# Kernel optimization log

Measured on AMD Instinct MI355X. Metric: run time of the kernel, lower is better.

The kernel has to match this reference:

```python
import jax, jax.numpy as jnp
import numpy as np

N = 100000
E = 640000
C = 128
NEG_SLOPE = 0.2


def _param(key, shape, scale=0.1):
    return jax.random.normal(key, shape, dtype=jnp.float32) * scale


def setup_inputs() -> dict:
    key = jax.random.key(0)
    ks = jax.random.split(key, 20)
    edge_index = jax.random.randint(ks[0], (2, E), 0, N, dtype=jnp.int32)
    emb = jax.random.normal(ks[1], (N, C), dtype=jnp.float32)  # node_embeddings.weight, a=1.0 normal
    d = {"edge_index": edge_index, "emb": emb}
    # per-layer GATv2Conv params: lin_l (W,b), lin_r (W,b), att vector, residual lin (no bias), out bias
    names = ["Wl", "bl", "Wr", "br", "att", "Wres", "bias"]
    shapes = [(C, C), (C,), (C, C), (C,), (C,), (C, C), (C,)]
    i = 2
    for layer in (1, 2):
        for nm, sh in zip(names, shapes):
            d[f"l{layer}_{nm}"] = _param(ks[i], sh)
            i += 1
    return d


def gatv2_layer(x, Wl, bl, Wr, br, att, Wres, bias, src, dst):
    # x: [N,C]; src/dst: [E+N] (self loops included)
    xl = x @ Wl.T + bl                       # source-side transform [N,C]
    xr = x @ Wr.T + br                       # target-side transform [N,C]
    m = jax.nn.leaky_relu(xl[src] + xr[dst], NEG_SLOPE)  # [E',C]
    e = m @ att                               # attention logits [E']
    emax = jax.ops.segment_max(e, dst, num_segments=N)
    ex = jnp.exp(e - emax[dst])
    denom = jax.ops.segment_sum(ex, dst, num_segments=N)
    alpha = ex / denom[dst]                   # segment softmax over incoming edges
    out = jax.ops.segment_sum(alpha[:, None] * xl[src], dst, num_segments=N)
    return out + x @ Wres.T + bias            # residual + bias


def reference(edge_index, emb,
              l1_Wl, l1_bl, l1_Wr, l1_br, l1_att, l1_Wres, l1_bias,
              l2_Wl, l2_bl, l2_Wr, l2_br, l2_att, l2_Wres, l2_bias):
    loops = jnp.arange(N, dtype=edge_index.dtype)
    src = jnp.concatenate([edge_index[0], loops])
    dst = jnp.concatenate([edge_index[1], loops])
    h = gatv2_layer(emb, l1_Wl, l1_bl, l1_Wr, l1_br, l1_att, l1_Wres, l1_bias, src, dst)
    h = jax.nn.relu(h)
    out = gatv2_layer(h, l2_Wl, l2_bl, l2_Wr, l2_br, l2_att, l2_Wres, l2_bias, src, dst)
    return out
```

## Files before the change

kernel.cpp:

```cpp
#include <hip/hip_runtime.h>
#include <math.h>

#define N_NODES 100000
#define N_EDGES 640000
#define C 128
#define CAP 32
#define N_TILES ((N_NODES + 63) / 64)

typedef __attribute__((ext_vector_type(8))) short short8;
typedef __attribute__((ext_vector_type(4))) float floatx4;
typedef __attribute__((ext_vector_type(2))) float float2v;
typedef unsigned int uint;
typedef unsigned short ushort;

__device__ __forceinline__ ushort f2bf(float f) {
    union { float f; uint u; } v; v.f = f;
    uint r = v.u + 0x7fffu + ((v.u >> 16) & 1u);
    return (ushort)(r >> 16);
}
__device__ __forceinline__ float2v upk2(uint u) {
    union { uint i; float f; } lo, hi;
    lo.i = u << 16; hi.i = u & 0xffff0000u;
    float2v r; r.x = lo.f; r.y = hi.f; return r;
}
__device__ __forceinline__ float2v fabs2(float2v v) {
    union { float2v f; uint u[2]; } a; a.f = v;
    a.u[0] &= 0x7fffffffu; a.u[1] &= 0x7fffffffu; return a.f;
}
__device__ __forceinline__ float2v fma2(float2v a, float2v b, float2v c) {
    return __builtin_elementwise_fma(a, b, c);
}

__device__ __forceinline__ float grp16_sum(float p) {
    union { float f; int i; } u, t;
    u.f = p;
    t.i = __builtin_amdgcn_update_dpp(0, u.i, 0xB1, 0xf, 0xf, true);  u.f += t.f;
    t.i = __builtin_amdgcn_update_dpp(0, u.i, 0x4E, 0xf, 0xf, true);  u.f += t.f;
    t.i = __builtin_amdgcn_update_dpp(0, u.i, 0x124, 0xf, 0xf, true); u.f += t.f;
    t.i = __builtin_amdgcn_update_dpp(0, u.i, 0x128, 0xf, 0xf, true); u.f += t.f;
    return u.f;
}

__global__ void prep_kernel(const float* __restrict__ w0, const float* __restrict__ w1,
                            const float* __restrict__ w2, const float* __restrict__ w3,
                            const float* __restrict__ w4, const float* __restrict__ w5,
                            ushort* __restrict__ wb, int* __restrict__ cnt) {
    const int bid = blockIdx.x;
    if (bid < 48) {
        int t = bid * 256 + threadIdx.x;
        int m = t >> 11;
        int off = (t & 2047) * 8;
        const float* src = (m == 0) ? w0 : (m == 1) ? w1 : (m == 2) ? w2
                          : (m == 3) ? w3 : (m == 4) ? w4 : w5;
        float4 v0 = *(const float4*)(src + off);
        float4 v1 = *(const float4*)(src + off + 4);
        ushort tmp[8];
        tmp[0] = f2bf(v0.x); tmp[1] = f2bf(v0.y); tmp[2] = f2bf(v0.z); tmp[3] = f2bf(v0.w);
        tmp[4] = f2bf(v1.x); tmp[5] = f2bf(v1.y); tmp[6] = f2bf(v1.z); tmp[7] = f2bf(v1.w);
        *(uint4*)(wb + (size_t)m * 16384 + off) = *(uint4*)tmp;
    } else {
        int idx = (bid - 48) * 256 + threadIdx.x;
        if (idx < N_NODES) cnt[idx] = 0;
    }
}

__global__ void build_kernel(const int* __restrict__ ei, int* __restrict__ cnt,
                             int* __restrict__ colsrc) {
    int i = blockIdx.x * 256 + threadIdx.x;
    if (i >= N_EDGES) return;
    int d = ei[N_EDGES + i];
    int s = ei[i];
    int slot = atomicAdd(&cnt[d], 1);
    if (slot < CAP) colsrc[(size_t)d * CAP + slot] = s;
}

template <int IN_F32, int RES_F32>
__global__ __launch_bounds__(512)
void gemm3_tile(const void* __restrict__ xin,
                const ushort* __restrict__ wb,
                const float* __restrict__ bl, const float* __restrict__ br,
                const float* __restrict__ bres,
                ushort* __restrict__ xl, ushort* __restrict__ xr,
                void* __restrict__ res) {
    __shared__ ushort xs[64][136];
    const int tid = threadIdx.x;
    const int wave = tid >> 6, lane = tid & 63;
    const int quad = lane >> 4, l16 = lane & 15;
    const int col = wave * 16 + l16;
    const int node = tid >> 3;
    const int kc = (tid & 7) * 16;

    const int tile = blockIdx.x;
    const int n = tile * 64 + node;

    ushort stg[16];
    if (n < N_NODES) {
        if (IN_F32) {
            const float* src = (const float*)xin + (size_t)n * C + kc;
            float4 v[4];
            #pragma unroll
            for (int i = 0; i < 4; ++i) v[i] = ((const float4*)src)[i];
            #pragma unroll
            for (int i = 0; i < 4; ++i) {
                stg[i * 4 + 0] = f2bf(v[i].x); stg[i * 4 + 1] = f2bf(v[i].y);
                stg[i * 4 + 2] = f2bf(v[i].z); stg[i * 4 + 3] = f2bf(v[i].w);
            }
        } else {
            const ushort* src = (const ushort*)xin + (size_t)n * C + kc;
            *(uint4*)&stg[0] = *(const uint4*)src;
            *(uint4*)&stg[8] = *(const uint4*)(src + 8);
        }
    } else {
        #pragma unroll
        for (int i = 0; i < 16; ++i) stg[i] = 0;
    }
    *(uint4*)&xs[node][kc]     = *(uint4*)&stg[0];
    *(uint4*)&xs[node][kc + 8] = *(uint4*)&stg[8];

    short8 bfr[3][4];
    #pragma unroll
    for (int ws = 0; ws < 3; ++ws)
        #pragma unroll
        for (int ks = 0; ks < 4; ++ks)
            bfr[ws][ks] = *(const short8*)(wb + (size_t)ws * 16384 + (size_t)col * 128 + ks * 32 + quad * 8);
    const float bias[3] = { bl[col], br[col], bres[col] };

    __syncthreads();

    floatx4 acc[4][3];
    #pragma unroll
    for (int rt = 0; rt < 4; ++rt)
        #pragma unroll
        for (int ws = 0; ws < 3; ++ws)
            acc[rt][ws] = (floatx4){0.f, 0.f, 0.f, 0.f};

    #pragma unroll
    for (int rt = 0; rt < 4; ++rt) {
        short8 a[4];
        #pragma unroll
        for (int ks = 0; ks < 4; ++ks)
            a[ks] = *(const short8*)&xs[rt * 16 + l16][ks * 32 + quad * 8];
        #pragma unroll
        for (int ws = 0; ws < 3; ++ws)
            #pragma unroll
            for (int ks = 0; ks < 4; ++ks)
                acc[rt][ws] = __builtin_amdgcn_mfma_f32_16x16x32_bf16(a[ks], bfr[ws][ks], acc[rt][ws], 0, 0, 0);
    }

    const int n0 = tile * 64;
    #pragma unroll
    for (int ws = 0; ws < 3; ++ws)
        #pragma unroll
        for (int rt = 0; rt < 4; ++rt)
            #pragma unroll
            for (int r = 0; r < 4; ++r) {
                int row = n0 + rt * 16 + quad * 4 + r;
                if (row < N_NODES) {
                    float val = acc[rt][ws][r] + bias[ws];
                    if (ws == 0)      xl[(size_t)row * C + col] = f2bf(val);
                    else if (ws == 1) xr[(size_t)row * C + col] = f2bf(val);
                    else if (RES_F32) ((float*)res)[(size_t)row * C + col] = val;
                    else              ((ushort*)res)[(size_t)row * C + col] = f2bf(val);
                }
            }
}

template <int OUT_BF16, int RELU, int RES_F32>
__global__ __launch_bounds__(256)
void node_kernel(const ushort* __restrict__ xl, const ushort* __restrict__ xr,
                 const float* __restrict__ att, const int* __restrict__ cnt,
                 const int* __restrict__ colsrc,
                 const void* __restrict__ resin, void* __restrict__ outp) {
    __shared__ int sdeg[16];
    __shared__ short smap[16];
    const int tid = threadIdx.x;

    if (tid < 16) sdeg[tid] = cnt[blockIdx.x * 16 + tid];
    __syncthreads();
    if (tid < 16) {
        const int my = sdeg[tid];
        int rank = 0;
        #pragma unroll
        for (int j = 0; j < 16; ++j) {
            const int dj = sdeg[j];
            rank += (int)((dj > my) | ((dj == my) & (j < tid)));
        }
        smap[rank] = (short)tid;
    }
    __syncthreads();

    const int gl = tid & 15;
    const int base_c = gl * 8;
    const int lidx = (int)smap[tid >> 4];
    const int d = blockIdx.x * 16 + lidx;
    const int deg0 = sdeg[lidx];

    float4 at0 = *(const float4*)(att + base_c);
    float4 at1 = *(const float4*)(att + base_c + 4);
    float2v a06[4], a04[4];
    a06[0] = (float2v){0.6f * at0.x, 0.6f * at0.y};
    a06[1] = (float2v){0.6f * at0.z, 0.6f * at0.w};
    a06[2] = (float2v){0.6f * at1.x, 0.6f * at1.y};
    a06[3] = (float2v){0.6f * at1.z, 0.6f * at1.w};
    a04[0] = (float2v){0.4f * at0.x, 0.4f * at0.y};
    a04[1] = (float2v){0.4f * at0.z, 0.4f * at0.w};
    a04[2] = (float2v){0.4f * at1.x, 0.4f * at1.y};
    a04[3] = (float2v){0.4f * at1.z, 0.4f * at1.w};

    uint4 uxr = *(const uint4*)(xr + (size_t)d * C + base_c);
    float2v xr2[4] = { upk2(uxr.x), upk2(uxr.y), upk2(uxr.z), upk2(uxr.w) };

    const int deg = (deg0 < CAP) ? deg0 : CAP;
    const int* cs = colsrc + (size_t)d * CAP;
    const int nch = (deg + 3) >> 2;

    uint4 selfraw = *(const uint4*)(xl + (size_t)d * C + base_c);

    auto xlrow = [&](int s) -> const uint4* {
        return (const uint4*)(xl + (((uint)s << 7) + (uint)base_c));
    };

    int4 sA = make_int4(d, d, d, d);
    if (deg > 0) sA = *(const int4*)cs;
    sA.x = (0 < deg) ? sA.x : d;
    sA.y = (1 < deg) ? sA.y : d;
    sA.z = (2 < deg) ? sA.z : d;
    sA.w = (3 < deg) ? sA.w : d;
    uint4 R0 = *xlrow(sA.x);
    uint4 R1 = *xlrow(sA.y);
    uint4 R2 = *xlrow(sA.z);
    uint4 R3 = *xlrow(sA.w);
    int4 sB = make_int4(d, d, d, d);
    if (deg > 4) sB = *(const int4*)(cs + 4);

    float S;
    float2v O2[4];

    {
        float2v xv[4] = { upk2(selfraw.x), upk2(selfraw.y), upk2(selfraw.z), upk2(selfraw.w) };
        float2v m0 = xv[0] + xr2[0];
        float2v m1 = xv[1] + xr2[1];
        float2v m2 = xv[2] + xr2[2];
        float2v m3 = xv[3] + xr2[3];
        float2v pa = fma2(a06[0], m0, a04[0] * fabs2(m0));
        float2v pb = fma2(a06[1], m1, a04[1] * fabs2(m1));
        pa = fma2(a06[2], m2, fma2(a04[2], fabs2(m2), pa));
        pb = fma2(a06[3], m3, fma2(a04[3], fabs2(m3), pb));
        pa += pb;
        float p = grp16_sum(pa.x + pa.y);
        const float w = __expf(p);
        S = w;
        float2v w2 = (float2v){w, w};
        #pragma unroll
        for (int j = 0; j < 4; ++j) O2[j] = w2 * xv[j];
    }

    for (int c = 0; c < nch; ++c) {
        const uint4 c0 = R0, c1 = R1, c2 = R2, c3 = R3;

        const int nb = (c + 1) * 4;
        int4 sN = sB;
        sN.x = (nb + 0 < deg) ? sN.x : d;
        sN.y = (nb + 1 < deg) ? sN.y : d;
        sN.z = (nb + 2 < deg) ? sN.z : d;
        sN.w = (nb + 3 < deg) ? sN.w : d;
        const int bb = (c + 2) * 4;
        if (bb < deg) sB = *(const int4*)(cs + bb);

        R0 = *xlrow(sN.x);
        R1 = *xlrow(sN.y);
        R2 = *xlrow(sN.z);
        R3 = *xlrow(sN.w);

        const int e0 = c * 4;
        const uint4 cur[4] = { c0, c1, c2, c3 };
        #pragma unroll
        for (int j = 0; j < 4; ++j) {
            float2v xv[4] = { upk2(cur[j].x), upk2(cur[j].y), upk2(cur[j].z), upk2(cur[j].w) };
            float2v m0 = xv[0] + xr2[0];
            float2v m1 = xv[1] + xr2[1];
            float2v m2 = xv[2] + xr2[2];
            float2v m3 = xv[3] + xr2[3];
            float2v pa = fma2(a06[0], m0, a04[0] * fabs2(m0));
            float2v pb = fma2(a06[1], m1, a04[1] * fabs2(m1));
            pa = fma2(a06[2], m2, fma2(a04[2], fabs2(m2), pa));
            pb = fma2(a06[3], m3, fma2(a04[3], fabs2(m3), pb));
            pa += pb;
            float p = grp16_sum(pa.x + pa.y);
            const float w = (e0 + j < deg) ? __expf(p) : 0.f;
            S += w;
            float2v w2 = (float2v){w, w};
            #pragma unroll
            for (int k = 0; k < 4; ++k) O2[k] = fma2(w2, xv[k], O2[k]);
        }
    }

    const float inv = 1.f / S;
    float2v rs[4];
    if (RES_F32) {
        const float* rp = (const float*)resin + (size_t)d * C + base_c;
        float4 q0 = *(const float4*)rp;
        float4 q1 = *(const float4*)(rp + 4);
        rs[0] = (float2v){q0.x, q0.y}; rs[1] = (float2v){q0.z, q0.w};
        rs[2] = (float2v){q1.x, q1.y}; rs[3] = (float2v){q1.z, q1.w};
    } else {
        uint4 urs = *(const uint4*)((const ushort*)resin + (size_t)d * C + base_c);
        rs[0] = upk2(urs.x); rs[1] = upk2(urs.y); rs[2] = upk2(urs.z); rs[3] = upk2(urs.w);
    }
    float2v iv = (float2v){inv, inv};
    float r[8];
    #pragma unroll
    for (int j = 0; j < 4; ++j) {
        float2v rr = fma2(O2[j], iv, rs[j]);
        if (RELU) { rr.x = fmaxf(rr.x, 0.f); rr.y = fmaxf(rr.y, 0.f); }
        r[2 * j] = rr.x; r[2 * j + 1] = rr.y;
    }
    if (OUT_BF16) {
        ushort tmp[8];
        #pragma unroll
        for (int c2 = 0; c2 < 8; ++c2) tmp[c2] = f2bf(r[c2]);
        *((uint4*)((ushort*)outp + (size_t)d * C + base_c)) = *(uint4*)tmp;
    } else {
        float* op = (float*)outp + (size_t)d * C + base_c;
        *(float4*)op       = make_float4(r[0], r[1], r[2], r[3]);
        *(float4*)(op + 4) = make_float4(r[4], r[5], r[6], r[7]);
    }
}

extern "C" void kernel_launch(void* const* d_in, const int* in_sizes, int n_in,
                              void* d_out, int out_size, void* d_ws, size_t ws_size,
                              hipStream_t stream) {
    const int*   ei  = (const int*)d_in[0];
    const float* emb = (const float*)d_in[1];
    const float* L1[7];
    const float* L2[7];
    for (int i = 0; i < 7; ++i) L1[i] = (const float*)d_in[2 + i];
    for (int i = 0; i < 7; ++i) L2[i] = (const float*)d_in[9 + i];
    float* out = (float*)d_out;

    const size_t NC = (size_t)N_NODES * C;
    ushort* xl  = (ushort*)d_ws;
    ushort* xr  = xl + NC;
    ushort* h   = xr + NC;
    ushort* wb  = h + NC;
    int* cnt    = (int*)(wb + 6 * 16384);
    int* colsrc = cnt + N_NODES;

    prep_kernel<<<48 + (N_NODES + 255) / 256, 256, 0, stream>>>(
        L1[0], L1[2], L1[5], L2[0], L2[2], L2[5], wb, cnt);
    build_kernel<<<(N_EDGES + 255) / 256, 256, 0, stream>>>(ei, cnt, colsrc);

    const int nblocks = N_NODES / 16;

    gemm3_tile<1, 0><<<N_TILES, 512, 0, stream>>>(emb, wb, L1[1], L1[3], L1[6], xl, xr, h);
    node_kernel<1, 1, 0><<<nblocks, 256, 0, stream>>>(xl, xr, L1[4], cnt, colsrc, h, h);

    gemm3_tile<0, 1><<<N_TILES, 512, 0, stream>>>(h, wb + 3 * 16384, L2[1], L2[3], L2[6], xl, xr, out);
    node_kernel<0, 0, 1><<<nblocks, 256, 0, stream>>>(xl, xr, L2[4], cnt, colsrc, out, out);
}
```

Baseline: 306.9 us.

## Fuse layer-1 aggregation with layer-2 projection GEMM in one node kernel

The layer-1 node aggregation kernel now keeps its 16 ReLU'd output rows in shared memory. It then runs the layer-2 Wl/Wr/Wres projections on them with bf16 MFMA instructions, which replaces the separate layer-2 GEMM launch and the round trip of h through global memory. The layer-2 xl/xr outputs reuse the old xr and h buffers. This is safe because each block only overwrites rows it has already read. The cost is that every block re-reads the full 96 KB of layer-2 weights and writes its outputs as scattered 2-byte stores, so cache and store efficiency may suffer.

```diff
diff --git a/kernel.cpp b/kernel.cpp
--- a/kernel.cpp
+++ b/kernel.cpp
@@ -165,14 +165,17 @@
             }
 }
 
-template <int OUT_BF16, int RELU, int RES_F32>
 __global__ __launch_bounds__(256)
-void node_kernel(const ushort* __restrict__ xl, const ushort* __restrict__ xr,
-                 const float* __restrict__ att, const int* __restrict__ cnt,
-                 const int* __restrict__ colsrc,
-                 const void* __restrict__ resin, void* __restrict__ outp) {
+void node_fused(const ushort* xl, const ushort* xr, const float* __restrict__ att,
+                const int* __restrict__ cnt, const int* __restrict__ colsrc,
+                const ushort* resin,
+                const ushort* __restrict__ wb2,
+                const float* __restrict__ bl2, const float* __restrict__ br2,
+                const float* __restrict__ bres2,
+                ushort* xl2out, ushort* xr2out, float* res2out) {
     __shared__ int sdeg[16];
     __shared__ short smap[16];
+    __shared__ ushort hs[16][136];
     const int tid = threadIdx.x;
 
     if (tid < 16) sdeg[tid] = cnt[blockIdx.x * 16 + tid];
@@ -192,7 +195,8 @@
     const int gl = tid & 15;
     const int base_c = gl * 8;
     const int lidx = (int)smap[tid >> 4];
-    const int d = blockIdx.x * 16 + lidx;
+    const int nb0 = blockIdx.x * 16;
+    const int d = nb0 + lidx;
     const int deg0 = sdeg[lidx];
 
     float4 at0 = *(const float4*)(att + base_c);
@@ -257,7 +261,6 @@
 
     for (int c = 0; c < nch; ++c) {
         const uint4 c0 = R0, c1 = R1, c2 = R2, c3 = R3;
-
         const int nb = (c + 1) * 4;
         int4 sN = sB;
         sN.x = (nb + 0 < deg) ? sN.x : d;
@@ -295,6 +298,191 @@
         }
     }
 
+    {
+        const float inv = 1.f / S;
+        uint4 urs = *(const uint4*)(resin + (size_t)d * C + base_c);
+        float2v rs[4] = { upk2(urs.x), upk2(urs.y), upk2(urs.z), upk2(urs.w) };
+        float2v iv = (float2v){inv, inv};
+        ushort tmp[8];
+        #pragma unroll
+        for (int j = 0; j < 4; ++j) {
+            float2v rr = fma2(O2[j], iv, rs[j]);
+            rr.x = fmaxf(rr.x, 0.f); rr.y = fmaxf(rr.y, 0.f);
+            tmp[2 * j]     = f2bf(rr.x);
+            tmp[2 * j + 1] = f2bf(rr.y);
+        }
+        *(uint4*)&hs[lidx][base_c] = *(uint4*)tmp;
+    }
+
+    __syncthreads();
+
+    const int wave = tid >> 6, lane = tid & 63;
+    const int quad = lane >> 4, l16 = lane & 15;
+
+    short8 a[4];
+    #pragma unroll
+    for (int ks = 0; ks < 4; ++ks)
+        a[ks] = *(const short8*)&hs[l16][ks * 32 + quad * 8];
+
+    #pragma unroll
+    for (int m = 0; m < 6; ++m) {
+        const int f0 = wave * 96 + m * 16;
+        const int wsI = f0 >> 7;
+        const int ch0 = f0 & 127;
+        const ushort* wp = wb2 + (size_t)wsI * 16384 + (size_t)(ch0 + l16) * 128 + quad * 8;
+        short8 bfr[4];
+        #pragma unroll
+        for (int ks = 0; ks < 4; ++ks)
+            bfr[ks] = *(const short8*)(wp + ks * 32);
+        floatx4 acc = (floatx4){0.f, 0.f, 0.f, 0.f};
+        #pragma unroll
+        for (int ks = 0; ks < 4; ++ks)
+            acc = __builtin_amdgcn_mfma_f32_16x16x32_bf16(a[ks], bfr[ks], acc, 0, 0, 0);
+
+        const float* bp = (wsI == 0) ? bl2 : (wsI == 1) ? br2 : bres2;
+        const int chn = ch0 + l16;
+        const float bias = bp[chn];
+        #pragma unroll
+        for (int r = 0; r < 4; ++r) {
+            const int node = nb0 + quad * 4 + r;
+            const float val = acc[r] + bias;
+            const size_t off = (size_t)node * C + chn;
+            if (wsI == 0)      xl2out[off] = f2bf(val);
+            else if (wsI == 1) xr2out[off] = f2bf(val);
+            else               res2out[off] = val;
+        }
+    }
+}
+
+template <int OUT_BF16, int RELU, int RES_F32>
+__global__ __launch_bounds__(256)
+void node_kernel(const ushort* xl, const ushort* xr,
+                 const float* __restrict__ att, const int* __restrict__ cnt,
+                 const int* __restrict__ colsrc,
+                 const void* resin, void* outp) {
+    __shared__ int sdeg[16];
+    __shared__ short smap[16];
+    const int tid = threadIdx.x;
+
+    if (tid < 16) sdeg[tid] = cnt[blockIdx.x * 16 + tid];
+    __syncthreads();
+    if (tid < 16) {
+        const int my = sdeg[tid];
+        int rank = 0;
+        #pragma unroll
+        for (int j = 0; j < 16; ++j) {
+            const int dj = sdeg[j];
+            rank += (int)((dj > my) | ((dj == my) & (j < tid)));
+        }
+        smap[rank] = (short)tid;
+    }
+    __syncthreads();
+
+    const int gl = tid & 15;
+    const int base_c = gl * 8;
+    const int lidx = (int)smap[tid >> 4];
+    const int d = blockIdx.x * 16 + lidx;
+    const int deg0 = sdeg[lidx];
+
+    float4 at0 = *(const float4*)(att + base_c);
+    float4 at1 = *(const float4*)(att + base_c + 4);
+    float2v a06[4], a04[4];
+    a06[0] = (float2v){0.6f * at0.x, 0.6f * at0.y};
+    a06[1] = (float2v){0.6f * at0.z, 0.6f * at0.w};
+    a06[2] = (float2v){0.6f * at1.x, 0.6f * at1.y};
+    a06[3] = (float2v){0.6f * at1.z, 0.6f * at1.w};
+    a04[0] = (float2v){0.4f * at0.x, 0.4f * at0.y};
+    a04[1] = (float2v){0.4f * at0.z, 0.4f * at0.w};
+    a04[2] = (float2v){0.4f * at1.x, 0.4f * at1.y};
+    a04[3] = (float2v){0.4f * at1.z, 0.4f * at1.w};
+
+    uint4 uxr = *(const uint4*)(xr + (size_t)d * C + base_c);
+    float2v xr2[4] = { upk2(uxr.x), upk2(uxr.y), upk2(uxr.z), upk2(uxr.w) };
+
+    const int deg = (deg0 < CAP) ? deg0 : CAP;
+    const int* cs = colsrc + (size_t)d * CAP;
+    const int nch = (deg + 3) >> 2;
+
+    uint4 selfraw = *(const uint4*)(xl + (size_t)d * C + base_c);
+
+    auto xlrow = [&](int s) -> const uint4* {
+        return (const uint4*)(xl + (((uint)s << 7) + (uint)base_c));
+    };
+
+    int4 sA = make_int4(d, d, d, d);
+    if (deg > 0) sA = *(const int4*)cs;
+    sA.x = (0 < deg) ? sA.x : d;
+    sA.y = (1 < deg) ? sA.y : d;
+    sA.z = (2 < deg) ? sA.z : d;
+    sA.w = (3 < deg) ? sA.w : d;
+    uint4 R0 = *xlrow(sA.x);
+    uint4 R1 = *xlrow(sA.y);
+    uint4 R2 = *xlrow(sA.z);
+    uint4 R3 = *xlrow(sA.w);
+    int4 sB = make_int4(d, d, d, d);
+    if (deg > 4) sB = *(const int4*)(cs + 4);
+
+    float S;
+    float2v O2[4];
+
+    {
+        float2v xv[4] = { upk2(selfraw.x), upk2(selfraw.y), upk2(selfraw.z), upk2(selfraw.w) };
+        float2v m0 = xv[0] + xr2[0];
+        float2v m1 = xv[1] + xr2[1];
+        float2v m2 = xv[2] + xr2[2];
+        float2v m3 = xv[3] + xr2[3];
+        float2v pa = fma2(a06[0], m0, a04[0] * fabs2(m0));
+        float2v pb = fma2(a06[1], m1, a04[1] * fabs2(m1));
+        pa = fma2(a06[2], m2, fma2(a04[2], fabs2(m2), pa));
+        pb = fma2(a06[3], m3, fma2(a04[3], fabs2(m3), pb));
+        pa += pb;
+        float p = grp16_sum(pa.x + pa.y);
+        const float w = __expf(p);
+        S = w;
+        float2v w2 = (float2v){w, w};
+        #pragma unroll
+        for (int j = 0; j < 4; ++j) O2[j] = w2 * xv[j];
+    }
+
+    for (int c = 0; c < nch; ++c) {
+        const uint4 c0 = R0, c1 = R1, c2 = R2, c3 = R3;
+        const int nb = (c + 1) * 4;
+        int4 sN = sB;
+        sN.x = (nb + 0 < deg) ? sN.x : d;
+        sN.y = (nb + 1 < deg) ? sN.y : d;
+        sN.z = (nb + 2 < deg) ? sN.z : d;
+        sN.w = (nb + 3 < deg) ? sN.w : d;
+        const int bb = (c + 2) * 4;
+        if (bb < deg) sB = *(const int4*)(cs + bb);
+
+        R0 = *xlrow(sN.x);
+        R1 = *xlrow(sN.y);
+        R2 = *xlrow(sN.z);
+        R3 = *xlrow(sN.w);
+
+        const int e0 = c * 4;
+        const uint4 cur[4] = { c0, c1, c2, c3 };
+        #pragma unroll
+        for (int j = 0; j < 4; ++j) {
+            float2v xv[4] = { upk2(cur[j].x), upk2(cur[j].y), upk2(cur[j].z), upk2(cur[j].w) };
+            float2v m0 = xv[0] + xr2[0];
+            float2v m1 = xv[1] + xr2[1];
+            float2v m2 = xv[2] + xr2[2];
+            float2v m3 = xv[3] + xr2[3];
+            float2v pa = fma2(a06[0], m0, a04[0] * fabs2(m0));
+            float2v pb = fma2(a06[1], m1, a04[1] * fabs2(m1));
+            pa = fma2(a06[2], m2, fma2(a04[2], fabs2(m2), pa));
+            pb = fma2(a06[3], m3, fma2(a04[3], fabs2(m3), pb));
+            pa += pb;
+            float p = grp16_sum(pa.x + pa.y);
+            const float w = (e0 + j < deg) ? __expf(p) : 0.f;
+            S += w;
+            float2v w2 = (float2v){w, w};
+            #pragma unroll
+            for (int k = 0; k < 4; ++k) O2[k] = fma2(w2, xv[k], O2[k]);
+        }
+    }
+
     const float inv = 1.f / S;
     float2v rs[4];
     if (RES_F32) {
@@ -353,8 +541,10 @@
     const int nblocks = N_NODES / 16;
 
     gemm3_tile<1, 0><<<N_TILES, 512, 0, stream>>>(emb, wb, L1[1], L1[3], L1[6], xl, xr, h);
-    node_kernel<1, 1, 0><<<nblocks, 256, 0, stream>>>(xl, xr, L1[4], cnt, colsrc, h, h);
-
-    gemm3_tile<0, 1><<<N_TILES, 512, 0, stream>>>(h, wb + 3 * 16384, L2[1], L2[3], L2[6], xl, xr, out);
-    node_kernel<0, 0, 1><<<nblocks, 256, 0, stream>>>(xl, xr, L2[4], cnt, colsrc, out, out);
-}
+
+    node_fused<<<nblocks, 256, 0, stream>>>(xl, xr, L1[4], cnt, colsrc, h,
+                                            wb + 3 * 16384, L2[1], L2[3], L2[6],
+                                            xr, h, out);
+
+    node_kernel<0, 0, 1><<<nblocks, 256, 0, stream>>>(xr, h, L2[4], cnt, colsrc, out, out);
+}
```

Result: slower. 339.7 us (+10.7%).

## Replace per-block node aggregation with persistent atomic work-queue kernel

Applied to the files above, without the earlier changes.

Replaces the fixed grid of 16-node blocks (which sorted nodes by degree within a block) with a persistent kernel of 2048 blocks where each wavefront grabs 4 destination nodes at a time via an atomic counter. The aim is dynamic load balancing across uneven in-degrees and less launch and tail overhead. In exchange it drops the in-block degree sorting, so the four nodes in a wavefront can have mismatched degrees and lanes may diverge. It also adds one global atomic per work item and two queue counters that prep_kernel resets.

```diff
diff --git a/kernel.cpp b/kernel.cpp
--- a/kernel.cpp
+++ b/kernel.cpp
@@ -6,6 +6,7 @@
 #define C 128
 #define CAP 32
 #define N_TILES ((N_NODES + 63) / 64)
+#define NQBLK 2048
 
 typedef __attribute__((ext_vector_type(8))) short short8;
 typedef __attribute__((ext_vector_type(4))) float floatx4;
@@ -44,7 +45,8 @@
 __global__ void prep_kernel(const float* __restrict__ w0, const float* __restrict__ w1,
                             const float* __restrict__ w2, const float* __restrict__ w3,
                             const float* __restrict__ w4, const float* __restrict__ w5,
-                            ushort* __restrict__ wb, int* __restrict__ cnt) {
+                            ushort* __restrict__ wb, int* __restrict__ cnt,
+                            int* __restrict__ qc) {
     const int bid = blockIdx.x;
     if (bid < 48) {
         int t = bid * 256 + threadIdx.x;
@@ -61,6 +63,7 @@
     } else {
         int idx = (bid - 48) * 256 + threadIdx.x;
         if (idx < N_NODES) cnt[idx] = 0;
+        if (idx < 2) qc[idx] = 0;
     }
 }
 
@@ -167,33 +170,15 @@
 
 template <int OUT_BF16, int RELU, int RES_F32>
 __global__ __launch_bounds__(256)
-void node_kernel(const ushort* __restrict__ xl, const ushort* __restrict__ xr,
-                 const float* __restrict__ att, const int* __restrict__ cnt,
-                 const int* __restrict__ colsrc,
-                 const void* __restrict__ resin, void* __restrict__ outp) {
-    __shared__ int sdeg[16];
-    __shared__ short smap[16];
+void node_queue(const ushort* xl, const ushort* xr,
+                const float* __restrict__ att, const int* __restrict__ cnt,
+                const int* __restrict__ colsrc,
+                const void* resin, void* outp, int* __restrict__ qhead) {
     const int tid = threadIdx.x;
-
-    if (tid < 16) sdeg[tid] = cnt[blockIdx.x * 16 + tid];
-    __syncthreads();
-    if (tid < 16) {
-        const int my = sdeg[tid];
-        int rank = 0;
-        #pragma unroll
-        for (int j = 0; j < 16; ++j) {
-            const int dj = sdeg[j];
-            rank += (int)((dj > my) | ((dj == my) & (j < tid)));
-        }
-        smap[rank] = (short)tid;
-    }
-    __syncthreads();
-
+    const int lane = tid & 63;
+    const int grp4 = (tid >> 4) & 3;
     const int gl = tid & 15;
     const int base_c = gl * 8;
-    const int lidx = (int)smap[tid >> 4];
-    const int d = blockIdx.x * 16 + lidx;
-    const int deg0 = sdeg[lidx];
 
     float4 at0 = *(const float4*)(att + base_c);
     float4 at1 = *(const float4*)(att + base_c + 4);
@@ -207,76 +192,45 @@
     a04[2] = (float2v){0.4f * at1.x, 0.4f * at1.y};
     a04[3] = (float2v){0.4f * at1.z, 0.4f * at1.w};
 
-    uint4 uxr = *(const uint4*)(xr + (size_t)d * C + base_c);
-    float2v xr2[4] = { upk2(uxr.x), upk2(uxr.y), upk2(uxr.z), upk2(uxr.w) };
-
-    const int deg = (deg0 < CAP) ? deg0 : CAP;
-    const int* cs = colsrc + (size_t)d * CAP;
-    const int nch = (deg + 3) >> 2;
-
-    uint4 selfraw = *(const uint4*)(xl + (size_t)d * C + base_c);
-
     auto xlrow = [&](int s) -> const uint4* {
         return (const uint4*)(xl + (((uint)s << 7) + (uint)base_c));
     };
 
-    int4 sA = make_int4(d, d, d, d);
-    if (deg > 0) sA = *(const int4*)cs;
-    sA.x = (0 < deg) ? sA.x : d;
-    sA.y = (1 < deg) ? sA.y : d;
-    sA.z = (2 < deg) ? sA.z : d;
-    sA.w = (3 < deg) ? sA.w : d;
-    uint4 R0 = *xlrow(sA.x);
-    uint4 R1 = *xlrow(sA.y);
-    uint4 R2 = *xlrow(sA.z);
-    uint4 R3 = *xlrow(sA.w);
-    int4 sB = make_int4(d, d, d, d);
-    if (deg > 4) sB = *(const int4*)(cs + 4);
-
-    float S;
-    float2v O2[4];
-
-    {
-        float2v xv[4] = { upk2(selfraw.x), upk2(selfraw.y), upk2(selfraw.z), upk2(selfraw.w) };
-        float2v m0 = xv[0] + xr2[0];
-        float2v m1 = xv[1] + xr2[1];
-        float2v m2 = xv[2] + xr2[2];
-        float2v m3 = xv[3] + xr2[3];
-        float2v pa = fma2(a06[0], m0, a04[0] * fabs2(m0));
-        float2v pb = fma2(a06[1], m1, a04[1] * fabs2(m1));
-        pa = fma2(a06[2], m2, fma2(a04[2], fabs2(m2), pa));
-        pb = fma2(a06[3], m3, fma2(a04[3], fabs2(m3), pb));
-        pa += pb;
-        float p = grp16_sum(pa.x + pa.y);
-        const float w = __expf(p);
-        S = w;
-        float2v w2 = (float2v){w, w};
-        #pragma unroll
-        for (int j = 0; j < 4; ++j) O2[j] = w2 * xv[j];
-    }
-
-    for (int c = 0; c < nch; ++c) {
-        const uint4 c0 = R0, c1 = R1, c2 = R2, c3 = R3;
-
-        const int nb = (c + 1) * 4;
-        int4 sN = sB;
-        sN.x = (nb + 0 < deg) ? sN.x : d;
-        sN.y = (nb + 1 < deg) ? sN.y : d;
-        sN.z = (nb + 2 < deg) ? sN.z : d;
-        sN.w = (nb + 3 < deg) ? sN.w : d;
-        const int bb = (c + 2) * 4;
-        if (bb < deg) sB = *(const int4*)(cs + bb);
-
-        R0 = *xlrow(sN.x);
-        R1 = *xlrow(sN.y);
-        R2 = *xlrow(sN.z);
-        R3 = *xlrow(sN.w);
-
-        const int e0 = c * 4;
-        const uint4 cur[4] = { c0, c1, c2, c3 };
-        #pragma unroll
-        for (int j = 0; j < 4; ++j) {
-            float2v xv[4] = { upk2(cur[j].x), upk2(cur[j].y), upk2(cur[j].z), upk2(cur[j].w) };
+    for (;;) {
+        int item;
+        if (lane == 0) item = atomicAdd(qhead, 1);
+        item = __builtin_amdgcn_readfirstlane(item);
+        const int nb = item * 4;
+        if (nb >= N_NODES) break;
+        const int d = nb + grp4;
+
+        const int deg0 = cnt[d];
+        const int deg = (deg0 < CAP) ? deg0 : CAP;
+        const int* cs = colsrc + (size_t)d * CAP;
+        const int nch = (deg + 3) >> 2;
+
+        uint4 uxr = *(const uint4*)(xr + (size_t)d * C + base_c);
+        float2v xr2[4] = { upk2(uxr.x), upk2(uxr.y), upk2(uxr.z), upk2(uxr.w) };
+        uint4 selfraw = *(const uint4*)(xl + (size_t)d * C + base_c);
+
+        int4 sA = make_int4(d, d, d, d);
+        if (deg > 0) sA = *(const int4*)cs;
+        sA.x = (0 < deg) ? sA.x : d;
+        sA.y = (1 < deg) ? sA.y : d;
+        sA.z = (2 < deg) ? sA.z : d;
+        sA.w = (3 < deg) ? sA.w : d;
+        uint4 R0 = *xlrow(sA.x);
+        uint4 R1 = *xlrow(sA.y);
+        uint4 R2 = *xlrow(sA.z);
+        uint4 R3 = *xlrow(sA.w);
+        int4 sB = make_int4(d, d, d, d);
+        if (deg > 4) sB = *(const int4*)(cs + 4);
+
+        float S;
+        float2v O2[4];
+
+        {
+            float2v xv[4] = { upk2(selfraw.x), upk2(selfraw.y), upk2(selfraw.z), upk2(selfraw.w) };
             float2v m0 = xv[0] + xr2[0];
             float2v m1 = xv[1] + xr2[1];
             float2v m2 = xv[2] + xr2[2];
@@ -287,43 +241,82 @@
             pb = fma2(a06[3], m3, fma2(a04[3], fabs2(m3), pb));
             pa += pb;
             float p = grp16_sum(pa.x + pa.y);
-            const float w = (e0 + j < deg) ? __expf(p) : 0.f;
-            S += w;
+            const float w = __expf(p);
+            S = w;
             float2v w2 = (float2v){w, w};
             #pragma unroll
-            for (int k = 0; k < 4; ++k) O2[k] = fma2(w2, xv[k], O2[k]);
-        }
-    }
-
-    const float inv = 1.f / S;
-    float2v rs[4];
-    if (RES_F32) {
-        const float* rp = (const float*)resin + (size_t)d * C + base_c;
-        float4 q0 = *(const float4*)rp;
-        float4 q1 = *(const float4*)(rp + 4);
-        rs[0] = (float2v){q0.x, q0.y}; rs[1] = (float2v){q0.z, q0.w};
-        rs[2] = (float2v){q1.x, q1.y}; rs[3] = (float2v){q1.z, q1.w};
-    } else {
-        uint4 urs = *(const uint4*)((const ushort*)resin + (size_t)d * C + base_c);
-        rs[0] = upk2(urs.x); rs[1] = upk2(urs.y); rs[2] = upk2(urs.z); rs[3] = upk2(urs.w);
-    }
-    float2v iv = (float2v){inv, inv};
-    float r[8];
-    #pragma unroll
-    for (int j = 0; j < 4; ++j) {
-        float2v rr = fma2(O2[j], iv, rs[j]);
-        if (RELU) { rr.x = fmaxf(rr.x, 0.f); rr.y = fmaxf(rr.y, 0.f); }
-        r[2 * j] = rr.x; r[2 * j + 1] = rr.y;
-    }
-    if (OUT_BF16) {
-        ushort tmp[8];
-        #pragma unroll
-        for (int c2 = 0; c2 < 8; ++c2) tmp[c2] = f2bf(r[c2]);
-        *((uint4*)((ushort*)outp + (size_t)d * C + base_c)) = *(uint4*)tmp;
-    } else {
-        float* op = (float*)outp + (size_t)d * C + base_c;
-        *(float4*)op       = make_float4(r[0], r[1], r[2], r[3]);
-        *(float4*)(op + 4) = make_float4(r[4], r[5], r[6], r[7]);
+            for (int j = 0; j < 4; ++j) O2[j] = w2 * xv[j];
+        }
+
+        for (int c = 0; c < nch; ++c) {
+            const uint4 c0 = R0, c1 = R1, c2 = R2, c3 = R3;
+            const int nbb = (c + 1) * 4;
+            int4 sN = sB;
+            sN.x = (nbb + 0 < deg) ? sN.x : d;
+            sN.y = (nbb + 1 < deg) ? sN.y : d;
+            sN.z = (nbb + 2 < deg) ? sN.z : d;
+            sN.w = (nbb + 3 < deg) ? sN.w : d;
+            const int bb = (c + 2) * 4;
+            if (bb < deg) sB = *(const int4*)(cs + bb);
+
+            R0 = *xlrow(sN.x);
+            R1 = *xlrow(sN.y);
+            R2 = *xlrow(sN.z);
+            R3 = *xlrow(sN.w);
+
+            const int e0 = c * 4;
+            const uint4 cur[4] = { c0, c1, c2, c3 };
+            #pragma unroll
+            for (int j = 0; j < 4; ++j) {
+                float2v xv[4] = { upk2(cur[j].x), upk2(cur[j].y), upk2(cur[j].z), upk2(cur[j].w) };
+                float2v m0 = xv[0] + xr2[0];
+                float2v m1 = xv[1] + xr2[1];
+                float2v m2 = xv[2] + xr2[2];
+                float2v m3 = xv[3] + xr2[3];
+                float2v pa = fma2(a06[0], m0, a04[0] * fabs2(m0));
+                float2v pb = fma2(a06[1], m1, a04[1] * fabs2(m1));
+                pa = fma2(a06[2], m2, fma2(a04[2], fabs2(m2), pa));
+                pb = fma2(a06[3], m3, fma2(a04[3], fabs2(m3), pb));
+                pa += pb;
+                float p = grp16_sum(pa.x + pa.y);
+                const float w = (e0 + j < deg) ? __expf(p) : 0.f;
+                S += w;
+                float2v w2 = (float2v){w, w};
+                #pragma unroll
+                for (int k = 0; k < 4; ++k) O2[k] = fma2(w2, xv[k], O2[k]);
+            }
+        }
+
+        const float inv = 1.f / S;
+        float2v rs[4];
+        if (RES_F32) {
+            const float* rp = (const float*)resin + (size_t)d * C + base_c;
+            float4 q0 = *(const float4*)rp;
+            float4 q1 = *(const float4*)(rp + 4);
+            rs[0] = (float2v){q0.x, q0.y}; rs[1] = (float2v){q0.z, q0.w};
+            rs[2] = (float2v){q1.x, q1.y}; rs[3] = (float2v){q1.z, q1.w};
+        } else {
+            uint4 urs = *(const uint4*)((const ushort*)resin + (size_t)d * C + base_c);
+            rs[0] = upk2(urs.x); rs[1] = upk2(urs.y); rs[2] = upk2(urs.z); rs[3] = upk2(urs.w);
+        }
+        float2v iv = (float2v){inv, inv};
+        float r[8];
+        #pragma unroll
+        for (int j = 0; j < 4; ++j) {
+            float2v rr = fma2(O2[j], iv, rs[j]);
+            if (RELU) { rr.x = fmaxf(rr.x, 0.f); rr.y = fmaxf(rr.y, 0.f); }
+            r[2 * j] = rr.x; r[2 * j + 1] = rr.y;
+        }
+        if (OUT_BF16) {
+            ushort tmp[8];
+            #pragma unroll
+            for (int c2 = 0; c2 < 8; ++c2) tmp[c2] = f2bf(r[c2]);
+            *((uint4*)((ushort*)outp + (size_t)d * C + base_c)) = *(uint4*)tmp;
+        } else {
+            float* op = (float*)outp + (size_t)d * C + base_c;
+            *(float4*)op       = make_float4(r[0], r[1], r[2], r[3]);
+            *(float4*)(op + 4) = make_float4(r[4], r[5], r[6], r[7]);
+        }
     }
 }
 
@@ -345,16 +338,15 @@
     ushort* wb  = h + NC;
     int* cnt    = (int*)(wb + 6 * 16384);
     int* colsrc = cnt + N_NODES;
+    int* qctr   = colsrc + (size_t)N_NODES * CAP;
 
     prep_kernel<<<48 + (N_NODES + 255) / 256, 256, 0, stream>>>(
-        L1[0], L1[2], L1[5], L2[0], L2[2], L2[5], wb, cnt);
+        L1[0], L1[2], L1[5], L2[0], L2[2], L2[5], wb, cnt, qctr);
     build_kernel<<<(N_EDGES + 255) / 256, 256, 0, stream>>>(ei, cnt, colsrc);
 
-    const int nblocks = N_NODES / 16;
-
     gemm3_tile<1, 0><<<N_TILES, 512, 0, stream>>>(emb, wb, L1[1], L1[3], L1[6], xl, xr, h);
-    node_kernel<1, 1, 0><<<nblocks, 256, 0, stream>>>(xl, xr, L1[4], cnt, colsrc, h, h);
+    node_queue<1, 1, 0><<<NQBLK, 256, 0, stream>>>(xl, xr, L1[4], cnt, colsrc, h, h, qctr);
 
     gemm3_tile<0, 1><<<N_TILES, 512, 0, stream>>>(h, wb + 3 * 16384, L2[1], L2[3], L2[6], xl, xr, out);
-    node_kernel<0, 0, 1><<<nblocks, 256, 0, stream>>>(xl, xr, L2[4], cnt, colsrc, out, out);
-}
+    node_queue<0, 0, 1><<<NQBLK, 256, 0, stream>>>(xl, xr, L2[4], cnt, colsrc, out, out, qctr + 1);
+}
```

After: 1.001 ms. 3.26x slower.
